# Kernel tuning notes

Hardware: AMD Instinct MI355X
Metric: run time of the kernel (lower is better)

Reference implementation:

```python
import jax, jax.numpy as jnp
import numpy as np

B, S, H = 2, 256, 2048
HK, HV, DK, DV, K = 16, 32, 128, 128, 4
KEY_DIM = HK * DK          # 2048
VAL_DIM = HV * DV          # 4096
CONV_DIM = 2 * KEY_DIM + VAL_DIM  # 8192
EPS = 1e-6


def setup_inputs() -> dict:
    key = jax.random.key(0)
    ks = jax.random.split(key, 10)
    s = 0.02
    return {
        "hidden_states": jax.random.normal(ks[0], (B, S, H), jnp.float32),
        "conv_state": jnp.zeros((B, CONV_DIM, K - 1), jnp.float32),
        "recurrent_state": jnp.zeros((B, HV, DK, DV), jnp.float32),
        "context_lengths": jnp.full((B,), S, jnp.int32),
        "W_qkv": jax.random.normal(ks[1], (H, CONV_DIM), jnp.float32) * s,
        "W_z": jax.random.normal(ks[2], (H, VAL_DIM), jnp.float32) * s,
        "W_b": jax.random.normal(ks[3], (H, HV), jnp.float32) * s,
        "W_a": jax.random.normal(ks[4], (H, HV), jnp.float32) * s,
        "conv_w": jax.random.normal(ks[5], (CONV_DIM, K), jnp.float32) * 0.1,
        "conv_b": jnp.zeros((CONV_DIM,), jnp.float32),
        "A_log": jax.random.normal(ks[6], (HV,), jnp.float32) * 0.1,
        "dt_bias": jnp.zeros((HV,), jnp.float32),
        "norm_w": jnp.ones((DV,), jnp.float32),
        "W_out": jax.random.normal(ks[7], (VAL_DIM, H), jnp.float32) * s,
    }


def _l2norm(x):
    return x * jax.lax.rsqrt(jnp.sum(x * x, axis=-1, keepdims=True) + EPS)


def reference(hidden_states, conv_state, recurrent_state, context_lengths,
              W_qkv, W_z, W_b, W_a, conv_w, conv_b, A_log, dt_bias,
              norm_w, W_out):
    # input projections
    mixed = hidden_states @ W_qkv            # [B,S,CONV_DIM]
    z = hidden_states @ W_z                  # [B,S,VAL_DIM]
    b = hidden_states @ W_b                  # [B,S,HV]
    a = hidden_states @ W_a                  # [B,S,HV]

    # stateful causal depthwise conv1d (kernel K, padding K-1)
    x_pad = jnp.concatenate([jnp.swapaxes(conv_state, 1, 2), mixed], axis=1)  # [B,S+K-1,C]
    conv_out = conv_b + sum(x_pad[:, j:j + S, :] * conv_w[:, j] for j in range(K))
    conv_state_out = jnp.swapaxes(x_pad[:, S:, :], 1, 2)  # last K-1 raw inputs [B,C,K-1]
    mixed = jax.nn.silu(conv_out)

    q, k, v = jnp.split(mixed, [KEY_DIM, 2 * KEY_DIM], axis=-1)
    q = _l2norm(q.reshape(B, S, HK, DK)) * (DK ** -0.5)
    k = _l2norm(k.reshape(B, S, HK, DK))
    v = v.reshape(B, S, HV, DV)
    # GQA-style repeat of key/query heads to value heads
    rep = HV // HK
    q = jnp.repeat(q, rep, axis=2)           # [B,S,HV,DK]
    k = jnp.repeat(k, rep, axis=2)

    # gating: log-decay g and write strength beta
    g = -jnp.exp(A_log) * jax.nn.softplus(a + dt_bias)  # [B,S,HV]
    beta = jax.nn.sigmoid(b)                            # [B,S,HV]

    # time-major for scan
    qs = jnp.swapaxes(q, 0, 1)   # [S,B,HV,DK]
    ks_ = jnp.swapaxes(k, 0, 1)
    vs = jnp.swapaxes(v, 0, 1)   # [S,B,HV,DV]
    gs = jnp.swapaxes(g, 0, 1)   # [S,B,HV]
    bs = jnp.swapaxes(beta, 0, 1)
    mask = jnp.arange(S)[:, None] < context_lengths[None, :]  # [S,B]

    def step(Sst, inp):
        qt, kt, vt, gt, bt, mt = inp
        Sd = Sst * jnp.exp(gt)[..., None, None]                # decay
        kv = jnp.einsum('bhk,bhkv->bhv', kt, Sd)               # prediction
        delta = (vt - kv) * bt[..., None]                      # delta-rule update
        Snew = Sd + jnp.einsum('bhk,bhv->bhkv', kt, delta)
        ot = jnp.einsum('bhk,bhkv->bhv', qt, Snew)
        Snew = jnp.where(mt[:, None, None, None], Snew, Sst)
        ot = jnp.where(mt[:, None, None], ot, 0.0)
        return Snew, ot

    Sfin, outs = jax.lax.scan(step, recurrent_state, (qs, ks_, vs, gs, bs, mask))
    o = jnp.swapaxes(outs, 0, 1)  # [B,S,HV,DV]

    # gated RMSNorm over value head dim
    o = o * jax.lax.rsqrt(jnp.mean(o * o, axis=-1, keepdims=True) + EPS) * norm_w
    o = o * jax.nn.silu(z.reshape(B, S, HV, DV))
    output = o.reshape(B, S, VAL_DIM) @ W_out
    return output, conv_state_out, Sfin
```

## Files before the change

kernel.cpp:

```cpp
#include <hip/hip_runtime.h>
#include <hip/hip_bf16.h>

#define BB     2
#define SEQ    256
#define HH     2048
#define HKc    16
#define HVc    32
#define DKc    128
#define DVc    128
#define KC     4
#define KEYD   2048
#define VALD   4096
#define CONVD  8192
#define MM     (BB*SEQ)
#define EPSf   1e-6f

typedef __attribute__((ext_vector_type(8))) short short8;
typedef __attribute__((ext_vector_type(4))) short short4v;
typedef __attribute__((ext_vector_type(4))) float floatx4;

__device__ __forceinline__ short f2bf(float f) {
  union { float f; unsigned u; } v; v.f = f;
  unsigned r = v.u + 0x7fffu + ((v.u >> 16) & 1u);
  return (short)(r >> 16);
}

__global__ __launch_bounds__(256) void trconv_kernel(
    const float* __restrict__ W, short* __restrict__ Wt, int K, int N) {
  __shared__ float ls[32][36];
  const int n0 = blockIdx.x * 32;
  const int k0 = blockIdx.y * 32;
  const int t = threadIdx.x;
  const int r = t >> 3, c4 = (t & 7) * 4;
  const float4 f = *(const float4*)&W[(size_t)(k0 + r) * N + n0 + c4];
  ls[r][c4] = f.x; ls[r][c4 + 1] = f.y; ls[r][c4 + 2] = f.z; ls[r][c4 + 3] = f.w;
  __syncthreads();
  short4v s;
  s[0] = f2bf(ls[c4 + 0][r]);
  s[1] = f2bf(ls[c4 + 1][r]);
  s[2] = f2bf(ls[c4 + 2][r]);
  s[3] = f2bf(ls[c4 + 3][r]);
  *(short4v*)&Wt[(size_t)(n0 + r) * K + k0 + c4] = s;
}

__global__ __launch_bounds__(256) void f2bf_kernel(
    const float* __restrict__ in, short* __restrict__ out) {
  const int i = blockIdx.x * 256 + threadIdx.x;
  const float4 a = *(const float4*)&in[(size_t)i * 8];
  const float4 b = *(const float4*)&in[(size_t)i * 8 + 4];
  short8 s;
  s[0] = f2bf(a.x); s[1] = f2bf(a.y); s[2] = f2bf(a.z); s[3] = f2bf(a.w);
  s[4] = f2bf(b.x); s[5] = f2bf(b.y); s[6] = f2bf(b.z); s[7] = f2bf(b.w);
  *(short8*)&out[(size_t)i * 8] = s;
}

#define PADs 40
__global__ __launch_bounds__(256) void gemm_bf16(
    const short* __restrict__ A, const short* __restrict__ Bt,
    float* __restrict__ C, int M, int N, int Kd, int lda) {
  __shared__ short As[64 * PADs];
  __shared__ short Bs[128 * PADs];
  const int tid = threadIdx.x;
  const int wave = tid >> 6, lane = tid & 63;
  const int wm = (wave >> 1) * 32, wn = (wave & 1) * 64;
  const int bm = blockIdx.y * 64, bn = blockIdx.x * 128;
  floatx4 acc[2][4] = {};
  const int sa_m = tid >> 2;
  const int sa_k = (tid & 3) * 8;
  const int fm = lane & 15, fq = (lane >> 4) * 8;
  const short* Ap  = A  + (size_t)(bm + sa_m) * lda + sa_k;
  const short* Bp0 = Bt + (size_t)(bn + sa_m) * Kd + sa_k;
  const short* Bp1 = Bt + (size_t)(bn + 64 + sa_m) * Kd + sa_k;
  short8 pa  = *(const short8*)(Ap);
  short8 pb0 = *(const short8*)(Bp0);
  short8 pb1 = *(const short8*)(Bp1);
  for (int k0 = 0; k0 < Kd; k0 += 32) {
    *(short8*)&As[sa_m * PADs + sa_k] = pa;
    *(short8*)&Bs[sa_m * PADs + sa_k] = pb0;
    *(short8*)&Bs[(64 + sa_m) * PADs + sa_k] = pb1;
    __syncthreads();
    if (k0 + 32 < Kd) {
      pa  = *(const short8*)(Ap + k0 + 32);
      pb0 = *(const short8*)(Bp0 + k0 + 32);
      pb1 = *(const short8*)(Bp1 + k0 + 32);
    }
    short8 af[2], bfr[4];
#pragma unroll
    for (int i = 0; i < 2; ++i)
      af[i] = *(const short8*)&As[(wm + i * 16 + fm) * PADs + fq];
#pragma unroll
    for (int j = 0; j < 4; ++j)
      bfr[j] = *(const short8*)&Bs[(wn + j * 16 + fm) * PADs + fq];
#pragma unroll
    for (int i = 0; i < 2; ++i)
#pragma unroll
      for (int j = 0; j < 4; ++j)
        acc[i][j] = __builtin_amdgcn_mfma_f32_16x16x32_bf16(af[i], bfr[j], acc[i][j], 0, 0, 0);
    __syncthreads();
  }
  const int cn = lane & 15, cr0 = (lane >> 4) * 4;
#pragma unroll
  for (int i = 0; i < 2; ++i)
#pragma unroll
    for (int j = 0; j < 4; ++j)
#pragma unroll
      for (int r = 0; r < 4; ++r)
        C[(size_t)(bm + wm + i * 16 + cr0 + r) * N + bn + wn + j * 16 + cn] = acc[i][j][r];
}

__global__ __launch_bounds__(256) void proj_ab_kernel(
    const float* __restrict__ hs, const float* __restrict__ Wb,
    const float* __restrict__ Wa, const float* __restrict__ A_log,
    const float* __restrict__ dt_bias, float* __restrict__ g_out,
    float* __restrict__ beta_out) {
  __shared__ float xs[HH];
  __shared__ float part[4][64];
  const int row = blockIdx.x;
  const int t = threadIdx.x;
  for (int i = t; i < HH; i += 256) xs[i] = hs[(size_t)row * HH + i];
  __syncthreads();
  const int j = t & 63;
  const int kc = t >> 6;
  const float* W = (j < 32) ? Wb : Wa;
  const int jj = j & 31;
  float p = 0.f;
  const int k0 = kc * 512;
#pragma unroll 8
  for (int k = k0; k < k0 + 512; ++k) p += xs[k] * W[k * 32 + jj];
  part[kc][j] = p;
  __syncthreads();
  if (t < 64) {
    float dot = part[0][t] + part[1][t] + part[2][t] + part[3][t];
    if (t < 32) {
      beta_out[row * HVc + t] = 1.f / (1.f + expf(-dot));
    } else {
      int h = t - 32;
      float x = dot + dt_bias[h];
      float sp = (x > 20.f) ? x : log1pf(expf(x));
      g_out[row * HVc + h] = -expf(A_log[h]) * sp;
    }
  }
}

#define CCH 16
__global__ __launch_bounds__(256) void conv_par_kernel(
    const float* __restrict__ mixed, const float* __restrict__ conv_state,
    const float* __restrict__ conv_w, const float* __restrict__ conv_b,
    float* __restrict__ cs) {
  const int c = blockIdx.x * 256 + threadIdx.x;
  const int s0 = blockIdx.y * CCH;
  const int b = blockIdx.z;
  const float4 w4 = *(const float4*)&conv_w[c * KC];
  const float bias = conv_b[c];
  float r0, r1, r2;
  if (s0 == 0) {
    size_t sb = (size_t)(b * CONVD + c) * (KC - 1);
    r0 = conv_state[sb + 0]; r1 = conv_state[sb + 1]; r2 = conv_state[sb + 2];
  } else {
    r0 = mixed[((size_t)(b * SEQ + s0 - 3)) * CONVD + c];
    r1 = mixed[((size_t)(b * SEQ + s0 - 2)) * CONVD + c];
    r2 = mixed[((size_t)(b * SEQ + s0 - 1)) * CONVD + c];
  }
#pragma unroll
  for (int s = s0; s < s0 + CCH; ++s) {
    size_t off = ((size_t)(b * SEQ + s)) * CONVD + c;
    float x = mixed[off];
    float acc = bias + r0 * w4.x + r1 * w4.y + r2 * w4.z + x * w4.w;
    cs[off] = acc / (1.f + expf(-acc));
    r0 = r1; r1 = r2; r2 = x;
  }
}

__global__ __launch_bounds__(256) void conv_state_out_kernel(
    const float* __restrict__ mixed, float* __restrict__ out2) {
  int idx = blockIdx.x * 256 + threadIdx.x;
  int t = idx % (KC - 1);
  int c = (idx / (KC - 1)) & (CONVD - 1);
  int b = idx / ((KC - 1) * CONVD);
  out2[idx] = mixed[((size_t)(b * SEQ + SEQ - (KC - 1) + t)) * CONVD + c];
}

__global__ __launch_bounds__(64) void l2norm_kernel(float* __restrict__ cs) {
  int bx = blockIdx.x;
  int which = bx & 1;
  int head = (bx >> 1) & 15;
  int row = bx >> 5;
  int lane = threadIdx.x;
  size_t base = (size_t)row * CONVD + (size_t)which * KEYD + head * DKc;
  float v0 = cs[base + lane];
  float v1 = cs[base + lane + 64];
  float ss = v0 * v0 + v1 * v1;
#pragma unroll
  for (int m = 1; m < 64; m <<= 1) ss += __shfl_xor(ss, m, 64);
  float rn = rsqrtf(ss + EPSf);
  if (!which) rn *= 0.08838834764831845f;
  cs[base + lane] = v0 * rn;
  cs[base + lane + 64] = v1 * rn;
}

#define SCH 8
__global__ __launch_bounds__(64, 2) void scan_kernel(
    const float* __restrict__ cs, const float* __restrict__ g_in,
    const float* __restrict__ beta_in, const float* __restrict__ rs0,
    const int* __restrict__ ctx, float* __restrict__ obuf,
    float* __restrict__ sftmp) {
  const int vg = blockIdx.x, h = blockIdx.y, b = blockIdx.z;
  const int bh = b * HVc + h;
  const int lane = threadIdx.x;
  const int kg = lane >> 2;
  const int c4 = lane & 3;
  const int col = vg * 4 + c4;
  const int khead = h >> 1;
  __shared__ float kl[2][SCH * 128];
  __shared__ float ql[2][SCH * 128];
  __shared__ float vl[2][SCH * 4];
  __shared__ float egl[2][SCH];
  __shared__ float btl[2][SCH];
  float S[8];
#pragma unroll
  for (int i = 0; i < 8; ++i)
    S[i] = rs0[((size_t)bh * DKc + kg * 8 + i) * DVc + col];
  const int cl = ctx[b];
  const size_t qgo = (size_t)khead * DKc;
  const size_t kgo = KEYD + (size_t)khead * DKc;
  const size_t vG = 2 * KEYD + (size_t)h * DVc + vg * 4;
  const size_t obase = ((size_t)bh * 32 + vg) * (SEQ * 4);
  const int r0g = b * SEQ;
  const int kg8 = kg * 8;
  float4 kreg[4], qreg[4], vreg;
  float egr = 0.f, btr = 0.f;
#pragma unroll
  for (int it = 0; it < 4; ++it) {
    int idx = it * 64 + lane, s = idx >> 5, d4 = idx & 31;
    const float* rp = cs + (size_t)(r0g + s) * CONVD;
    kreg[it] = *(const float4*)(rp + kgo + d4 * 4);
    qreg[it] = *(const float4*)(rp + qgo + d4 * 4);
  }
  if (lane < 8)       vreg = *(const float4*)(cs + (size_t)(r0g + lane) * CONVD + vG);
  else if (lane < 16) egr = expf(g_in[(r0g + lane - 8) * HVc + h]);
  else if (lane < 24) btr = beta_in[(r0g + lane - 16) * HVc + h];
#pragma unroll
  for (int it = 0; it < 4; ++it) {
    int idx = it * 64 + lane, s = idx >> 5, d4 = idx & 31;
    *(float4*)&kl[0][s * 128 + d4 * 4] = kreg[it];
    *(float4*)&ql[0][s * 128 + d4 * 4] = qreg[it];
  }
  if (lane < 8)       *(float4*)&vl[0][lane * 4] = vreg;
  else if (lane < 16) egl[0][lane - 8] = egr;
  else if (lane < 24) btl[0][lane - 16] = btr;

  const int NCH = SEQ / SCH;
  for (int c = 0; c < NCH; ++c) {
    const int buf = c & 1;
    if (c + 1 < NCH) {
      const int r1 = r0g + (c + 1) * SCH;
#pragma unroll
      for (int it = 0; it < 4; ++it) {
        int idx = it * 64 + lane, s = idx >> 5, d4 = idx & 31;
        const float* rp = cs + (size_t)(r1 + s) * CONVD;
        kreg[it] = *(const float4*)(rp + kgo + d4 * 4);
        qreg[it] = *(const float4*)(rp + qgo + d4 * 4);
      }
      if (lane < 8)       vreg = *(const float4*)(cs + (size_t)(r1 + lane) * CONVD + vG);
      else if (lane < 16) egr = expf(g_in[(r1 + lane - 8) * HVc + h]);
      else if (lane < 24) btr = beta_in[(r1 + lane - 16) * HVc + h];
    }
#pragma unroll
    for (int s = 0; s < SCH; ++s) {
      const int sg = c * SCH + s;
      const float eg = egl[buf][s], bt = btl[buf][s];
      const float vv = vl[buf][s * 4 + c4];
      const float4* k4 = (const float4*)&kl[buf][s * 128 + kg8];
      const float4* q4 = (const float4*)&ql[buf][s * 128 + kg8];
      if (sg < cl) {
        const float4 kk0 = k4[0], kk1 = k4[1];
        float a0, a1, a2, a3;
        S[0] *= eg; a0 = kk0.x * S[0];
        S[1] *= eg; a1 = kk0.y * S[1];
        S[2] *= eg; a2 = kk0.z * S[2];
        S[3] *= eg; a3 = kk0.w * S[3];
        S[4] *= eg; a0 += kk1.x * S[4];
        S[5] *= eg; a1 += kk1.y * S[5];
        S[6] *= eg; a2 += kk1.z * S[6];
        S[7] *= eg; a3 += kk1.w * S[7];
        float p = (a0 + a1) + (a2 + a3);
        p += __shfl_xor(p, 4, 64);
        p += __shfl_xor(p, 8, 64);
        p += __shfl_xor(p, 16, 64);
        p += __shfl_xor(p, 32, 64);
        const float delta = (vv - p) * bt;
        const float4 qq0 = q4[0], qq1 = q4[1];
        float o0, o1, o2, o3;
        S[0] += kk0.x * delta; o0 = qq0.x * S[0];
        S[1] += kk0.y * delta; o1 = qq0.y * S[1];
        S[2] += kk0.z * delta; o2 = qq0.z * S[2];
        S[3] += kk0.w * delta; o3 = qq0.w * S[3];
        S[4] += kk1.x * delta; o0 += qq1.x * S[4];
        S[5] += kk1.y * delta; o1 += qq1.y * S[5];
        S[6] += kk1.z * delta; o2 += qq1.z * S[6];
        S[7] += kk1.w * delta; o3 += qq1.w * S[7];
        float o = (o0 + o1) + (o2 + o3);
        o += __shfl_xor(o, 4, 64);
        o += __shfl_xor(o, 8, 64);
        o += __shfl_xor(o, 16, 64);
        o += __shfl_xor(o, 32, 64);
        if (kg == 0) obuf[obase + sg * 4 + c4] = o;
      } else {
        if (kg == 0) obuf[obase + sg * 4 + c4] = 0.f;
      }
    }
    if (c + 1 < NCH) {
      const int nb = buf ^ 1;
#pragma unroll
      for (int it = 0; it < 4; ++it) {
        int idx = it * 64 + lane, s = idx >> 5, d4 = idx & 31;
        *(float4*)&kl[nb][s * 128 + d4 * 4] = kreg[it];
        *(float4*)&ql[nb][s * 128 + d4 * 4] = qreg[it];
      }
      if (lane < 8)       *(float4*)&vl[nb][lane * 4] = vreg;
      else if (lane < 16) egl[nb][lane - 8] = egr;
      else if (lane < 24) btl[nb][lane - 16] = btr;
    }
  }
  const size_t sb = (((size_t)bh * 32 + vg) * DKc + kg8) * 4 + c4;
#pragma unroll
  for (int i = 0; i < 8; ++i)
    sftmp[sb + i * 4] = S[i];
}

__global__ __launch_bounds__(128) void sfin_tr_kernel(
    const float* __restrict__ sftmp, float* __restrict__ out_sf) {
  const int dk = blockIdx.x;
  const int bh = blockIdx.y;
  const int dv = threadIdx.x;
  out_sf[((size_t)bh * DKc + dk) * DVc + dv] =
      sftmp[(((size_t)bh * 32 + (dv >> 2)) * DKc + dk) * 4 + (dv & 3)];
}

__global__ __launch_bounds__(64) void normgate_kernel(
    const float* __restrict__ obuf, const float* __restrict__ zbuf,
    const float* __restrict__ norm_w, short* __restrict__ o16) {
  int bx = blockIdx.x;
  int h = bx & 31;
  int row = bx >> 5;
  int b = row >> 8;
  int s = row & (SEQ - 1);
  int lane = threadIdx.x;
  size_t ob = ((size_t)(b * HVc + h) * 32 + (lane >> 2)) * (SEQ * 4) + s * 4 + (lane & 3);
  size_t zb = (size_t)row * VALD + h * DVc;
  float o0 = obuf[ob];
  float o1 = obuf[ob + 16 * (SEQ * 4)];
  float ss = o0 * o0 + o1 * o1;
#pragma unroll
  for (int m = 1; m < 64; m <<= 1) ss += __shfl_xor(ss, m, 64);
  float rms = rsqrtf(ss * (1.f / 128.f) + EPSf);
  float z0 = zbuf[zb + lane];
  float z1 = zbuf[zb + lane + 64];
  o16[zb + lane]      = f2bf(o0 * rms * norm_w[lane]      * (z0 / (1.f + expf(-z0))));
  o16[zb + lane + 64] = f2bf(o1 * rms * norm_w[lane + 64] * (z1 / (1.f + expf(-z1))));
}

extern "C" void kernel_launch(void* const* d_in, const int* in_sizes, int n_in,
                              void* d_out, int out_size, void* d_ws, size_t ws_size,
                              hipStream_t stream) {
  const float* hs        = (const float*)d_in[0];
  const float* conv_st   = (const float*)d_in[1];
  const float* rec_st    = (const float*)d_in[2];
  const int*   ctx       = (const int*)d_in[3];
  const float* W_qkv     = (const float*)d_in[4];
  const float* W_z       = (const float*)d_in[5];
  const float* W_b       = (const float*)d_in[6];
  const float* W_a       = (const float*)d_in[7];
  const float* conv_w    = (const float*)d_in[8];
  const float* conv_b    = (const float*)d_in[9];
  const float* A_log     = (const float*)d_in[10];
  const float* dt_bias   = (const float*)d_in[11];
  const float* norm_w    = (const float*)d_in[12];
  const float* W_out     = (const float*)d_in[13];

  float* out0   = (float*)d_out;
  float* out_cv = out0 + (size_t)MM * HH;
  float* out_sf = out_cv + (size_t)BB * CONVD * (KC - 1);

  char*  base  = (char*)d_ws;
  float* mixed = (float*)base;
  char*  wtB   = base + (size_t)MM * CONVD * 4;
  short* wt    = (short*)wtB;
  float* cs    = (float*)wtB;
  float* zbuf  = (float*)(wtB + (size_t)MM * CONVD * 4);
  float* gbuf  = (float*)(wtB + (size_t)CONVD * HH * 2);
  float* betab = gbuf + (size_t)MM * HVc;
  short* hs16  = (short*)(betab + (size_t)MM * HVc);
  short* o16   = hs16 + (size_t)MM * HH;
  float* obuf  = mixed;
  float* sftmp = mixed + (size_t)MM * VALD;

  f2bf_kernel<<<(MM * HH / 8) / 256, 256, 0, stream>>>(hs, hs16);
  trconv_kernel<<<dim3(CONVD / 32, HH / 32), 256, 0, stream>>>(W_qkv, wt, HH, CONVD);
  gemm_bf16<<<dim3(CONVD / 128, MM / 64), 256, 0, stream>>>(hs16, wt, mixed, MM, CONVD, HH, HH);
  trconv_kernel<<<dim3(VALD / 32, HH / 32), 256, 0, stream>>>(W_z, wt, HH, VALD);
  gemm_bf16<<<dim3(VALD / 128, MM / 64), 256, 0, stream>>>(hs16, wt, zbuf, MM, VALD, HH, HH);
  proj_ab_kernel<<<MM, 256, 0, stream>>>(hs, W_b, W_a, A_log, dt_bias, gbuf, betab);
  conv_par_kernel<<<dim3(CONVD / 256, SEQ / CCH, BB), 256, 0, stream>>>(
      mixed, conv_st, conv_w, conv_b, cs);
  conv_state_out_kernel<<<(BB * CONVD * (KC - 1)) / 256, 256, 0, stream>>>(mixed, out_cv);
  l2norm_kernel<<<MM * HKc * 2, 64, 0, stream>>>(cs);
  scan_kernel<<<dim3(32, HVc, BB), 64, 0, stream>>>(cs, gbuf, betab, rec_st, ctx, obuf, sftmp);
  sfin_tr_kernel<<<dim3(DKc, BB * HVc), 128, 0, stream>>>(sftmp, out_sf);
  normgate_kernel<<<MM * HVc, 64, 0, stream>>>(obuf, zbuf, norm_w, o16);
  trconv_kernel<<<dim3(HH / 32, VALD / 32), 256, 0, stream>>>(W_out, wt, VALD, HH);
  gemm_bf16<<<dim3(HH / 128, MM / 64), 256, 0, stream>>>(o16, wt, out0, MM, HH, VALD, VALD);
}
```

Before: 515.3 us.

## Replace LDS double-buffered chunk staging in scan with direct register prefetch

The recurrent scan kernel no longer stages k/q/v/gate/beta chunks through double-buffered shared memory. Each lane now loads its own 8-element k and q slices, v, exp(g) and beta straight from global memory into registers, two timesteps ahead in a ping-pong scheme. This removes the LDS writes and reads and the per-chunk staging work from the serial critical path. In exchange there are more redundant global loads across lanes (many lanes in a wave read the same k/q data, relying on cache), and only two steps of prefetch depth may not hide global latency.

```diff
diff --git a/kernel.cpp b/kernel.cpp
--- a/kernel.cpp
+++ b/kernel.cpp
@@ -198,7 +198,14 @@
   cs[base + lane + 64] = v1 * rn;
 }
 
-#define SCH 8
+__device__ __forceinline__ float red_kg(float x) {
+  x += __shfl_xor(x, 4, 64);
+  x += __shfl_xor(x, 8, 64);
+  x += __shfl_xor(x, 16, 64);
+  x += __shfl_xor(x, 32, 64);
+  return x;
+}
+
 __global__ __launch_bounds__(64, 2) void scan_kernel(
     const float* __restrict__ cs, const float* __restrict__ g_in,
     const float* __restrict__ beta_in, const float* __restrict__ rs0,
@@ -211,117 +218,70 @@
   const int c4 = lane & 3;
   const int col = vg * 4 + c4;
   const int khead = h >> 1;
-  __shared__ float kl[2][SCH * 128];
-  __shared__ float ql[2][SCH * 128];
-  __shared__ float vl[2][SCH * 4];
-  __shared__ float egl[2][SCH];
-  __shared__ float btl[2][SCH];
   float S[8];
 #pragma unroll
   for (int i = 0; i < 8; ++i)
     S[i] = rs0[((size_t)bh * DKc + kg * 8 + i) * DVc + col];
   const int cl = ctx[b];
-  const size_t qgo = (size_t)khead * DKc;
-  const size_t kgo = KEYD + (size_t)khead * DKc;
-  const size_t vG = 2 * KEYD + (size_t)h * DVc + vg * 4;
+  const int kg8 = kg * 8;
+  const size_t qgo = (size_t)khead * DKc + kg8;
+  const size_t kgo = KEYD + (size_t)khead * DKc + kg8;
+  const size_t vGc = 2 * KEYD + (size_t)h * DVc + vg * 4 + c4;
   const size_t obase = ((size_t)bh * 32 + vg) * (SEQ * 4);
   const int r0g = b * SEQ;
-  const int kg8 = kg * 8;
-  float4 kreg[4], qreg[4], vreg;
-  float egr = 0.f, btr = 0.f;
-#pragma unroll
-  for (int it = 0; it < 4; ++it) {
-    int idx = it * 64 + lane, s = idx >> 5, d4 = idx & 31;
-    const float* rp = cs + (size_t)(r0g + s) * CONVD;
-    kreg[it] = *(const float4*)(rp + kgo + d4 * 4);
-    qreg[it] = *(const float4*)(rp + qgo + d4 * 4);
-  }
-  if (lane < 8)       vreg = *(const float4*)(cs + (size_t)(r0g + lane) * CONVD + vG);
-  else if (lane < 16) egr = expf(g_in[(r0g + lane - 8) * HVc + h]);
-  else if (lane < 24) btr = beta_in[(r0g + lane - 16) * HVc + h];
-#pragma unroll
-  for (int it = 0; it < 4; ++it) {
-    int idx = it * 64 + lane, s = idx >> 5, d4 = idx & 31;
-    *(float4*)&kl[0][s * 128 + d4 * 4] = kreg[it];
-    *(float4*)&ql[0][s * 128 + d4 * 4] = qreg[it];
-  }
-  if (lane < 8)       *(float4*)&vl[0][lane * 4] = vreg;
-  else if (lane < 16) egl[0][lane - 8] = egr;
-  else if (lane < 24) btl[0][lane - 16] = btr;
-
-  const int NCH = SEQ / SCH;
-  for (int c = 0; c < NCH; ++c) {
-    const int buf = c & 1;
-    if (c + 1 < NCH) {
-      const int r1 = r0g + (c + 1) * SCH;
-#pragma unroll
-      for (int it = 0; it < 4; ++it) {
-        int idx = it * 64 + lane, s = idx >> 5, d4 = idx & 31;
-        const float* rp = cs + (size_t)(r1 + s) * CONVD;
-        kreg[it] = *(const float4*)(rp + kgo + d4 * 4);
-        qreg[it] = *(const float4*)(rp + qgo + d4 * 4);
-      }
-      if (lane < 8)       vreg = *(const float4*)(cs + (size_t)(r1 + lane) * CONVD + vG);
-      else if (lane < 16) egr = expf(g_in[(r1 + lane - 8) * HVc + h]);
-      else if (lane < 24) btr = beta_in[(r1 + lane - 16) * HVc + h];
-    }
-#pragma unroll
-    for (int s = 0; s < SCH; ++s) {
-      const int sg = c * SCH + s;
-      const float eg = egl[buf][s], bt = btl[buf][s];
-      const float vv = vl[buf][s * 4 + c4];
-      const float4* k4 = (const float4*)&kl[buf][s * 128 + kg8];
-      const float4* q4 = (const float4*)&ql[buf][s * 128 + kg8];
-      if (sg < cl) {
-        const float4 kk0 = k4[0], kk1 = k4[1];
-        float a0, a1, a2, a3;
-        S[0] *= eg; a0 = kk0.x * S[0];
-        S[1] *= eg; a1 = kk0.y * S[1];
-        S[2] *= eg; a2 = kk0.z * S[2];
-        S[3] *= eg; a3 = kk0.w * S[3];
-        S[4] *= eg; a0 += kk1.x * S[4];
-        S[5] *= eg; a1 += kk1.y * S[5];
-        S[6] *= eg; a2 += kk1.z * S[6];
-        S[7] *= eg; a3 += kk1.w * S[7];
-        float p = (a0 + a1) + (a2 + a3);
-        p += __shfl_xor(p, 4, 64);
-        p += __shfl_xor(p, 8, 64);
-        p += __shfl_xor(p, 16, 64);
-        p += __shfl_xor(p, 32, 64);
-        const float delta = (vv - p) * bt;
-        const float4 qq0 = q4[0], qq1 = q4[1];
-        float o0, o1, o2, o3;
-        S[0] += kk0.x * delta; o0 = qq0.x * S[0];
-        S[1] += kk0.y * delta; o1 = qq0.y * S[1];
-        S[2] += kk0.z * delta; o2 = qq0.z * S[2];
-        S[3] += kk0.w * delta; o3 = qq0.w * S[3];
-        S[4] += kk1.x * delta; o0 += qq1.x * S[4];
-        S[5] += kk1.y * delta; o1 += qq1.y * S[5];
-        S[6] += kk1.z * delta; o2 += qq1.z * S[6];
-        S[7] += kk1.w * delta; o3 += qq1.w * S[7];
-        float o = (o0 + o1) + (o2 + o3);
-        o += __shfl_xor(o, 4, 64);
-        o += __shfl_xor(o, 8, 64);
-        o += __shfl_xor(o, 16, 64);
-        o += __shfl_xor(o, 32, 64);
-        if (kg == 0) obuf[obase + sg * 4 + c4] = o;
-      } else {
-        if (kg == 0) obuf[obase + sg * 4 + c4] = 0.f;
-      }
-    }
-    if (c + 1 < NCH) {
-      const int nb = buf ^ 1;
-#pragma unroll
-      for (int it = 0; it < 4; ++it) {
-        int idx = it * 64 + lane, s = idx >> 5, d4 = idx & 31;
-        *(float4*)&kl[nb][s * 128 + d4 * 4] = kreg[it];
-        *(float4*)&ql[nb][s * 128 + d4 * 4] = qreg[it];
-      }
-      if (lane < 8)       *(float4*)&vl[nb][lane * 4] = vreg;
-      else if (lane < 16) egl[nb][lane - 8] = egr;
-      else if (lane < 24) btl[nb][lane - 16] = btr;
-    }
-  }
+
+#define SCAN_LOADS(s_, K0, K1, Q0, Q1, V, EG, BT) {                        \
+    const int sc_ = ((s_) < SEQ) ? (s_) : (SEQ - 1);                       \
+    const float* rp_ = cs + (size_t)(r0g + sc_) * CONVD;                   \
+    K0 = *(const float4*)(rp_ + kgo);                                      \
+    K1 = *(const float4*)(rp_ + kgo + 4);                                  \
+    Q0 = *(const float4*)(rp_ + qgo);                                      \
+    Q1 = *(const float4*)(rp_ + qgo + 4);                                  \
+    V  = rp_[vGc];                                                         \
+    EG = expf(g_in[(r0g + sc_) * HVc + h]);                                \
+    BT = beta_in[(r0g + sc_) * HVc + h]; }
+
+#define SCAN_STEP(kk0, kk1, qq0, qq1, vv, eg, bt, sg_) {                   \
+    if ((sg_) < cl) {                                                      \
+      float a0, a1, a2, a3;                                                \
+      S[0] *= eg; a0 = kk0.x * S[0];                                       \
+      S[1] *= eg; a1 = kk0.y * S[1];                                       \
+      S[2] *= eg; a2 = kk0.z * S[2];                                       \
+      S[3] *= eg; a3 = kk0.w * S[3];                                       \
+      S[4] *= eg; a0 += kk1.x * S[4];                                      \
+      S[5] *= eg; a1 += kk1.y * S[5];                                      \
+      S[6] *= eg; a2 += kk1.z * S[6];                                      \
+      S[7] *= eg; a3 += kk1.w * S[7];                                      \
+      float p = red_kg((a0 + a1) + (a2 + a3));                             \
+      const float delta = (vv - p) * bt;                                   \
+      float o0, o1, o2, o3;                                                \
+      S[0] += kk0.x * delta; o0 = qq0.x * S[0];                            \
+      S[1] += kk0.y * delta; o1 = qq0.y * S[1];                            \
+      S[2] += kk0.z * delta; o2 = qq0.z * S[2];                            \
+      S[3] += kk0.w * delta; o3 = qq0.w * S[3];                            \
+      S[4] += kk1.x * delta; o0 += qq1.x * S[4];                           \
+      S[5] += kk1.y * delta; o1 += qq1.y * S[5];                           \
+      S[6] += kk1.z * delta; o2 += qq1.z * S[6];                           \
+      S[7] += kk1.w * delta; o3 += qq1.w * S[7];                           \
+      float o = red_kg((o0 + o1) + (o2 + o3));                             \
+      if (kg == 0) obuf[obase + (sg_) * 4 + c4] = o;                       \
+    } else {                                                               \
+      if (kg == 0) obuf[obase + (sg_) * 4 + c4] = 0.f;                     \
+    } }
+
+  float4 kA0, kA1, qA0, qA1; float vA, egA, btA;
+  float4 kB0, kB1, qB0, qB1; float vB, egB, btB;
+  SCAN_LOADS(0, kA0, kA1, qA0, qA1, vA, egA, btA);
+  SCAN_LOADS(1, kB0, kB1, qB0, qB1, vB, egB, btB);
+  for (int s = 0; s < SEQ; s += 2) {
+    SCAN_STEP(kA0, kA1, qA0, qA1, vA, egA, btA, s);
+    SCAN_LOADS(s + 2, kA0, kA1, qA0, qA1, vA, egA, btA);
+    SCAN_STEP(kB0, kB1, qB0, qB1, vB, egB, btB, s + 1);
+    SCAN_LOADS(s + 3, kB0, kB1, qB0, qB1, vB, egB, btB);
+  }
+#undef SCAN_LOADS
+#undef SCAN_STEP
+
   const size_t sb = (((size_t)bh * 32 + vg) * DKc + kg8) * 4 + c4;
 #pragma unroll
   for (int i = 0; i < 8; ++i)
```

Result: slower. 548.3 us (+6.4%).

## Add split-K with atomic accumulation to projection GEMMs and widen weight transpose tiles

Applied to the files above, without the earlier changes.

The bf16 GEMM gains a K-split grid dimension. Partial products are accumulated into pre-zeroed fp32 outputs with atomicAdd. The QKV and z projections use 2 splits and the output projection uses 4, to fill more compute units, especially for the small-N output GEMM. The weight transpose/convert kernel now handles 64 K-rows per block and writes 8-wide bf16 vectors. This adds zero-fill kernels and atomic traffic, and makes the fp32 summation order nondeterministic.

```diff
diff --git a/kernel.cpp b/kernel.cpp
--- a/kernel.cpp
+++ b/kernel.cpp
@@ -25,22 +25,31 @@
   return (short)(r >> 16);
 }
 
+__global__ __launch_bounds__(256) void zerof_kernel(float* __restrict__ p) {
+  float4 z; z.x = 0.f; z.y = 0.f; z.z = 0.f; z.w = 0.f;
+  *(float4*)&p[(size_t)(blockIdx.x * 256 + threadIdx.x) * 4] = z;
+}
+
 __global__ __launch_bounds__(256) void trconv_kernel(
     const float* __restrict__ W, short* __restrict__ Wt, int K, int N) {
-  __shared__ float ls[32][36];
+  __shared__ float ls[64][33];
   const int n0 = blockIdx.x * 32;
-  const int k0 = blockIdx.y * 32;
+  const int k0 = blockIdx.y * 64;
   const int t = threadIdx.x;
-  const int r = t >> 3, c4 = (t & 7) * 4;
-  const float4 f = *(const float4*)&W[(size_t)(k0 + r) * N + n0 + c4];
-  ls[r][c4] = f.x; ls[r][c4 + 1] = f.y; ls[r][c4 + 2] = f.z; ls[r][c4 + 3] = f.w;
+#pragma unroll
+  for (int it = 0; it < 2; ++it) {
+    const int kr = (t >> 3) + it * 32;
+    const int c4 = (t & 7) * 4;
+    const float4 f = *(const float4*)&W[(size_t)(k0 + kr) * N + n0 + c4];
+    ls[kr][c4] = f.x; ls[kr][c4 + 1] = f.y; ls[kr][c4 + 2] = f.z; ls[kr][c4 + 3] = f.w;
+  }
   __syncthreads();
-  short4v s;
-  s[0] = f2bf(ls[c4 + 0][r]);
-  s[1] = f2bf(ls[c4 + 1][r]);
-  s[2] = f2bf(ls[c4 + 2][r]);
-  s[3] = f2bf(ls[c4 + 3][r]);
-  *(short4v*)&Wt[(size_t)(n0 + r) * K + k0 + c4] = s;
+  const int r = t >> 3;
+  const int kc = (t & 7) * 8;
+  short8 s;
+#pragma unroll
+  for (int j = 0; j < 8; ++j) s[j] = f2bf(ls[kc + j][r]);
+  *(short8*)&Wt[(size_t)(n0 + r) * K + k0 + kc] = s;
 }
 
 __global__ __launch_bounds__(256) void f2bf_kernel(
@@ -57,29 +66,30 @@
 #define PADs 40
 __global__ __launch_bounds__(256) void gemm_bf16(
     const short* __restrict__ A, const short* __restrict__ Bt,
-    float* __restrict__ C, int M, int N, int Kd, int lda) {
+    float* __restrict__ C, int M, int N, int Kd, int lda, int klen, int atom) {
   __shared__ short As[64 * PADs];
   __shared__ short Bs[128 * PADs];
   const int tid = threadIdx.x;
   const int wave = tid >> 6, lane = tid & 63;
   const int wm = (wave >> 1) * 32, wn = (wave & 1) * 64;
   const int bm = blockIdx.y * 64, bn = blockIdx.x * 128;
+  const int koff = blockIdx.z * klen;
   floatx4 acc[2][4] = {};
   const int sa_m = tid >> 2;
   const int sa_k = (tid & 3) * 8;
   const int fm = lane & 15, fq = (lane >> 4) * 8;
-  const short* Ap  = A  + (size_t)(bm + sa_m) * lda + sa_k;
-  const short* Bp0 = Bt + (size_t)(bn + sa_m) * Kd + sa_k;
-  const short* Bp1 = Bt + (size_t)(bn + 64 + sa_m) * Kd + sa_k;
+  const short* Ap  = A  + (size_t)(bm + sa_m) * lda + koff + sa_k;
+  const short* Bp0 = Bt + (size_t)(bn + sa_m) * Kd + koff + sa_k;
+  const short* Bp1 = Bt + (size_t)(bn + 64 + sa_m) * Kd + koff + sa_k;
   short8 pa  = *(const short8*)(Ap);
   short8 pb0 = *(const short8*)(Bp0);
   short8 pb1 = *(const short8*)(Bp1);
-  for (int k0 = 0; k0 < Kd; k0 += 32) {
+  for (int k0 = 0; k0 < klen; k0 += 32) {
     *(short8*)&As[sa_m * PADs + sa_k] = pa;
     *(short8*)&Bs[sa_m * PADs + sa_k] = pb0;
     *(short8*)&Bs[(64 + sa_m) * PADs + sa_k] = pb1;
     __syncthreads();
-    if (k0 + 32 < Kd) {
+    if (k0 + 32 < klen) {
       pa  = *(const short8*)(Ap + k0 + 32);
       pb0 = *(const short8*)(Bp0 + k0 + 32);
       pb1 = *(const short8*)(Bp1 + k0 + 32);
@@ -99,13 +109,24 @@
     __syncthreads();
   }
   const int cn = lane & 15, cr0 = (lane >> 4) * 4;
-#pragma unroll
-  for (int i = 0; i < 2; ++i)
-#pragma unroll
-    for (int j = 0; j < 4; ++j)
-#pragma unroll
-      for (int r = 0; r < 4; ++r)
-        C[(size_t)(bm + wm + i * 16 + cr0 + r) * N + bn + wn + j * 16 + cn] = acc[i][j][r];
+  if (atom) {
+#pragma unroll
+    for (int i = 0; i < 2; ++i)
+#pragma unroll
+      for (int j = 0; j < 4; ++j)
+#pragma unroll
+        for (int r = 0; r < 4; ++r)
+          atomicAdd(&C[(size_t)(bm + wm + i * 16 + cr0 + r) * N + bn + wn + j * 16 + cn],
+                    acc[i][j][r]);
+  } else {
+#pragma unroll
+    for (int i = 0; i < 2; ++i)
+#pragma unroll
+      for (int j = 0; j < 4; ++j)
+#pragma unroll
+        for (int r = 0; r < 4; ++r)
+          C[(size_t)(bm + wm + i * 16 + cr0 + r) * N + bn + wn + j * 16 + cn] = acc[i][j][r];
+  }
 }
 
 __global__ __launch_bounds__(256) void proj_ab_kernel(
@@ -396,10 +417,14 @@
   float* sftmp = mixed + (size_t)MM * VALD;
 
   f2bf_kernel<<<(MM * HH / 8) / 256, 256, 0, stream>>>(hs, hs16);
-  trconv_kernel<<<dim3(CONVD / 32, HH / 32), 256, 0, stream>>>(W_qkv, wt, HH, CONVD);
-  gemm_bf16<<<dim3(CONVD / 128, MM / 64), 256, 0, stream>>>(hs16, wt, mixed, MM, CONVD, HH, HH);
-  trconv_kernel<<<dim3(VALD / 32, HH / 32), 256, 0, stream>>>(W_z, wt, HH, VALD);
-  gemm_bf16<<<dim3(VALD / 128, MM / 64), 256, 0, stream>>>(hs16, wt, zbuf, MM, VALD, HH, HH);
+  trconv_kernel<<<dim3(CONVD / 32, HH / 64), 256, 0, stream>>>(W_qkv, wt, HH, CONVD);
+  zerof_kernel<<<(MM * CONVD / 4) / 256, 256, 0, stream>>>(mixed);
+  gemm_bf16<<<dim3(CONVD / 128, MM / 64, 2), 256, 0, stream>>>(
+      hs16, wt, mixed, MM, CONVD, HH, HH, HH / 2, 1);
+  trconv_kernel<<<dim3(VALD / 32, HH / 64), 256, 0, stream>>>(W_z, wt, HH, VALD);
+  zerof_kernel<<<(MM * VALD / 4) / 256, 256, 0, stream>>>(zbuf);
+  gemm_bf16<<<dim3(VALD / 128, MM / 64, 2), 256, 0, stream>>>(
+      hs16, wt, zbuf, MM, VALD, HH, HH, HH / 2, 1);
   proj_ab_kernel<<<MM, 256, 0, stream>>>(hs, W_b, W_a, A_log, dt_bias, gbuf, betab);
   conv_par_kernel<<<dim3(CONVD / 256, SEQ / CCH, BB), 256, 0, stream>>>(
       mixed, conv_st, conv_w, conv_b, cs);
@@ -408,6 +433,8 @@
   scan_kernel<<<dim3(32, HVc, BB), 64, 0, stream>>>(cs, gbuf, betab, rec_st, ctx, obuf, sftmp);
   sfin_tr_kernel<<<dim3(DKc, BB * HVc), 128, 0, stream>>>(sftmp, out_sf);
   normgate_kernel<<<MM * HVc, 64, 0, stream>>>(obuf, zbuf, norm_w, o16);
-  trconv_kernel<<<dim3(HH / 32, VALD / 32), 256, 0, stream>>>(W_out, wt, VALD, HH);
-  gemm_bf16<<<dim3(HH / 128, MM / 64), 256, 0, stream>>>(o16, wt, out0, MM, HH, VALD, VALD);
-}
+  trconv_kernel<<<dim3(HH / 32, VALD / 64), 256, 0, stream>>>(W_out, wt, VALD, HH);
+  zerof_kernel<<<(MM * HH / 4) / 256, 256, 0, stream>>>(out0);
+  gemm_bf16<<<dim3(HH / 128, MM / 64, 4), 256, 0, stream>>>(
+      o16, wt, out0, MM, HH, VALD, VALD, VALD / 4, 1);
+}
```

After: 517.9 us. No clear change (+0.5%).
